# Performance work log

Measured on AMD Instinct MI355X. Metric: run time of the kernel, lower is better.

The kernel has to match this reference:

```python
import jax, jax.numpy as jnp
import numpy as np

NEG = -1e30  # log-space 'zero'


def _lse3(a, b, c):
    # numerically stable logsumexp of three [B,L] arrays, NEG acts as -inf
    m = jnp.maximum(jnp.maximum(a, b), c)
    valid = m > NEG / 2
    m_safe = jnp.where(valid, m, 0.0)
    s = jnp.exp(a - m_safe) + jnp.exp(b - m_safe) + jnp.exp(c - m_safe)
    # add 1 where invalid so log() stays finite (result is masked anyway)
    return jnp.where(valid, m_safe + jnp.log(s + (~valid)), NEG)


def _lse2(a, b):
    m = jnp.maximum(a, b)
    valid = m > NEG / 2
    m_safe = jnp.where(valid, m, 0.0)
    s = jnp.exp(a - m_safe) + jnp.exp(b - m_safe)
    return jnp.where(valid, m_safe + jnp.log(s + (~valid)), NEG)


def ctc_loss(log_probs, targets, input_lengths, target_lengths):
    # log_probs: [T,B,C] already log-softmaxed; blank=0; reduction='mean'; zero_infinity
    T, B, C = log_probs.shape
    S = targets.shape[0] // B  # equal target lengths -> reshape concatenated targets
    tgt = targets.reshape(B, S)
    L = 2 * S + 1
    # extended label sequence: blank, l1, blank, l2, ..., blank
    ext = jnp.zeros((B, L), dtype=tgt.dtype).at[:, 1::2].set(tgt)
    # emissions gathered at extended labels: [T,B,L]
    emit = log_probs[:, jnp.arange(B)[:, None], ext]

    # skip transition (l-2 -> l) allowed iff ext[l] != blank and ext[l] != ext[l-2]
    skip_ok = jnp.concatenate(
        [jnp.zeros((B, 2), bool), (ext[:, 2:] != 0) & (ext[:, 2:] != ext[:, :-2])],
        axis=1,
    )

    def shift(a, n):
        return jnp.pad(a, ((0, 0), (n, 0)), constant_values=NEG)[:, :L]

    alpha0 = (
        jnp.full((B, L), NEG, log_probs.dtype)
        .at[:, 0].set(emit[0, :, 0])
        .at[:, 1].set(emit[0, :, 1])
    )

    def step(alpha, xs):
        t, emit_t = xs
        a1 = shift(alpha, 1)
        a2 = jnp.where(skip_ok, shift(alpha, 2), NEG)
        new = _lse3(alpha, a1, a2) + emit_t
        # freeze alpha once past each sample's input length
        new = jnp.where((t < input_lengths)[:, None], new, alpha)
        return new, None

    alpha, _ = jax.lax.scan(step, alpha0, (jnp.arange(1, T), emit[1:]))

    b_idx = jnp.arange(B)
    hi = 2 * target_lengths  # last blank position
    ll = _lse2(alpha[b_idx, hi], alpha[b_idx, hi - 1])
    loss = jnp.where(ll > NEG / 2, -ll, 0.0)  # zero_infinity=True
    return jnp.mean(loss / target_lengths.astype(log_probs.dtype))


def setup_inputs() -> dict:
    key = jax.random.key(0)
    k1, k2 = jax.random.split(key)
    T, B, C, S = 1024, 128, 256, 64
    logits = jax.random.normal(k1, (T, B, C), jnp.float32)
    log_probs = jax.nn.log_softmax(logits, axis=-1)
    targets = jax.random.randint(k2, (B * S,), 1, C)  # blank=0 excluded
    input_lengths = jnp.full((B,), T, jnp.int32)
    target_lengths = jnp.full((B,), S, jnp.int32)
    return {
        "log_probs": log_probs,
        "targets": targets,
        "input_lengths": input_lengths,
        "target_lengths": target_lengths,
    }


def reference(log_probs, targets, input_lengths, target_lengths):
    return ctc_loss(log_probs, targets, input_lengths, target_lengths)
```

## Files before the change

kernel.cpp:

```cpp
#include <hip/hip_runtime.h>


#define NEGV (-1e30f)
#define NEGH (-5e29f)

constexpr int T_  = 1024;
constexpr int C_  = 256;
constexpr int CH  = 64;
constexpr int NCH = T_ / CH;

__device__ __forceinline__ float lse2f(float x, float y) {
    float m = fmaxf(x, y);
    float s = __expf(x - m) + __expf(y - m);
    float r = m + __logf(s);
    return (m > NEGH) ? r : NEGV;
}

__device__ __forceinline__ float fshr1(float x) {
    int i = __float_as_int(x);
    int p = __builtin_amdgcn_update_dpp(0, i, 0x138, 0xf, 0xf, false);
    return __int_as_float(p);
}

template <int CTRL>
__device__ __forceinline__ int dpp_imaxstep(int x) {
    int r = __builtin_amdgcn_update_dpp(x, x, CTRL, 0xf, 0xf, false);
    return max(x, r);
}

#define PDECL(S) float S##g0,S##g1,S##g2,S##g3,S##g4,S##g5,S##g6,S##g7, \
                       S##l0,S##l1,S##l2,S##l3,S##l4,S##l5,S##l6,S##l7
#define PLOAD1(S,J,TB) { int t_ = (TB) + J; t_ = t_ > 1023 ? 1023 : t_;      \
    const float* rp_ = rowb + (size_t)t_ * BC;                               \
    S##g##J = rp_[my_tgt]; S##l##J = rp_[0]; }
#define PLOAD(S,TB) PLOAD1(S,0,TB) PLOAD1(S,1,TB) PLOAD1(S,2,TB)             \
                    PLOAD1(S,3,TB) PLOAD1(S,4,TB) PLOAD1(S,5,TB)             \
                    PLOAD1(S,6,TB) PLOAD1(S,7,TB)
#define PSTORE1(S,J,RB,BUFP) BUFP[((RB) + J) * 64 + lane] =                  \
    make_float2(__expf(S##g##J), __expf(S##l##J));
#define PSTORE(S,RB,BUFP) PSTORE1(S,0,RB,BUFP) PSTORE1(S,1,RB,BUFP)          \
                          PSTORE1(S,2,RB,BUFP) PSTORE1(S,3,RB,BUFP)          \
                          PSTORE1(S,4,RB,BUFP) PSTORE1(S,5,RB,BUFP)          \
                          PSTORE1(S,6,RB,BUFP) PSTORE1(S,7,RB,BUFP)
#define LOADCHUNK(T0) PLOAD(A,(T0)) PLOAD(Bx,(T0)+8)                         \
                      PLOAD(Cx,(T0)+16) PLOAD(Dx,(T0)+24)
#define STORECHUNK(RB,BUFP) PSTORE(A,(RB),BUFP) PSTORE(Bx,(RB)+8,BUFP)       \
                            PSTORE(Cx,(RB)+16,BUFP) PSTORE(Dx,(RB)+24,BUFP)

__global__ __launch_bounds__(192) void ctc_alpha_kernel(
    const float* __restrict__ lp,
    const int* __restrict__ targets,
    const int* __restrict__ in_len,
    const int* __restrict__ tgt_len,
    float* __restrict__ partial,
    int B, int S)
{
    __shared__ float2 stage[2][CH * 64];
    __shared__ float sh[132];

    const int b    = blockIdx.x;
    const int tid  = threadIdx.x;
    const int wave = tid >> 6;
    const int lane = tid & 63;
    const int BC   = B * C_;
    const float* rowb = lp + (size_t)b * C_;

    int my_tgt = (lane < S) ? targets[b * S + lane] : 0;
    int prev_tgt = __shfl_up(my_tgt, 1);
    const bool skip = (lane > 0) && (my_tgt != prev_tgt) && (my_tgt != 0);
    const float skipf = skip ? 1.f : 0.f;
    const int ilen = in_len[b];

    float pa = 0.f, pb = 0.f, pc = 0.f;
    int es = 0;

    PDECL(A); PDECL(Bx); PDECL(Cx); PDECL(Dx);
    const int r0 = (wave - 1) * 32;

    if (wave >= 1) {
        LOADCHUNK(1 + r0);
        { float2* bp = &stage[0][0]; STORECHUNK(r0, bp); }
        LOADCHUNK(1 + CH + r0);
    } else if (lane == 0) {
        pa = __expf(rowb[0]);
        pb = __expf(rowb[my_tgt]);
    }
    __syncthreads();

#define STEP(cur) {                                                          \
        float eml = (cur).x;                                                 \
        float ebl = (cur).y;                                                 \
        float pprev = fshr1(pb);                                \
        float t0s = pa + pb;                               \
        float nb = fmaf(skipf, pprev, t0s) * eml;            \
        float na = (pa + pprev) * ebl;                       \
        float nc = (pc + pb) * ebl;                          \
        pa = na; pb = nb; pc = nc; }

#define RESCALE() {                                                          \
        int h = __float_as_int(fmaxf(fmaxf(pa, pb), pc));                    \
        h = dpp_imaxstep<0x111>(h);                         \
        h = dpp_imaxstep<0x112>(h);                         \
        h = dpp_imaxstep<0x114>(h);                         \
        h = dpp_imaxstep<0x118>(h);                         \
        h = dpp_imaxstep<0x142>(h);                         \
        h = dpp_imaxstep<0x143>(h);                         \
        int hm = __builtin_amdgcn_readlane(h, 63);                           \
        int e = ((hm >> 23) & 0xff) - 127;                                   \
        pa = ldexpf(pa, -e); pb = ldexpf(pb, -e); pc = ldexpf(pc, -e);       \
        es += e; }

    for (int kc = 0; kc < NCH; ++kc) {
        if (wave >= 1) {
            if (kc + 1 < NCH) {
                float2* bp = &stage[(kc + 1) & 1][0];
                STORECHUNK(r0, bp);
            }
            if (kc + 2 < NCH) {
                LOADCHUNK(1 + (kc + 2) * CH + r0);
            }
        } else {
            const int t0 = 1 + kc * CH;
            const float2* sb = &stage[kc & 1][lane];
            if (t0 + CH <= ilen) {
                float2 f0 = sb[0 * 64];
                float2 f1 = sb[1 * 64];
                float2 f2 = sb[2 * 64];
                float2 f3 = sb[3 * 64];
#pragma unroll
                for (int r = 0; r < CH; ++r) {
                    float2 cur = f0;
                    f0 = f1; f1 = f2; f2 = f3;
                    if (r + 4 < CH) f3 = sb[(r + 4) * 64];
                    STEP(cur);
                    if ((r & 7) == 7) RESCALE();
                }
            } else if (t0 < ilen) {
                float2 f0 = sb[0 * 64];
                float2 f1 = sb[1 * 64];
                float2 f2 = sb[2 * 64];
                float2 f3 = sb[3 * 64];
#pragma unroll
                for (int r = 0; r < CH; ++r) {
                    float2 cur = f0;
                    f0 = f1; f1 = f2; f2 = f3;
                    if (r + 4 < CH) f3 = sb[(r + 4) * 64];
                    if (t0 + r < ilen) {
                        STEP(cur);
                        if ((r & 7) == 7) RESCALE();
                    }
                }
            }
        }
        __syncthreads();
    }

    if (wave == 0) {
        const double lses = (double)es * 0.6931471805599453;
        auto logp = [&](float p) -> float {
            if (p == 0.f) return NEGV;
            float q = p * 33554432.0f;
            if (q == 0.f) return NEGV;
            int h = __float_as_int(q);
            int E = ((h >> 23) & 0xff) - 127 - 25;
            float m = __int_as_float((h & 0x807fffff) | (127 << 23));
            return (float)(__logf(m) + ((double)E * 0.6931471805599453 + lses));
        };
        sh[2 * lane]     = logp(pa);
        sh[2 * lane + 1] = logp(pb);
        if (lane == 63) sh[128] = logp(pc);
    }
    __syncthreads();
    if (tid == 0) {
        int tl = tgt_len[b];
        int hi2 = 2 * tl;
        float ll = lse2f(sh[hi2], sh[hi2 - 1]);
        float loss = (ll > NEGH) ? -ll : 0.f;
        partial[b] = loss / (float)tl;
    }
}

__global__ __launch_bounds__(128) void ctc_reduce_kernel(
    const float* __restrict__ partial, float* __restrict__ out, int B)
{
    float v = 0.f;
    for (int j = threadIdx.x; j < B; j += 128) v += partial[j];
#pragma unroll
    for (int off = 32; off > 0; off >>= 1)
        v += __shfl_down(v, off);
    __shared__ float ws[2];
    if ((threadIdx.x & 63) == 0) ws[threadIdx.x >> 6] = v;
    __syncthreads();
    if (threadIdx.x == 0) out[0] = (ws[0] + ws[1]) / (float)B;
}

extern "C" void kernel_launch(void* const* d_in, const int* in_sizes, int n_in,
                              void* d_out, int out_size, void* d_ws, size_t ws_size,
                              hipStream_t stream)
{
    const float* lp      = (const float*)d_in[0];
    const int*   targets = (const int*)d_in[1];
    const int*   il      = (const int*)d_in[2];
    const int*   tl      = (const int*)d_in[3];
    const int B = in_sizes[2];
    const int S = in_sizes[1] / B;

    float* partial = (float*)d_ws;

    ctc_alpha_kernel<<<B, 192, 0, stream>>>(lp, targets, il, tl, partial, B, S);
    ctc_reduce_kernel<<<1, 128, 0, stream>>>(partial, (float*)d_out, B);
}
```

Baseline: 195.1 us.

## Use per-lane scale exponents instead of wave-wide max rescaling

Replaces the wave-wide max reduction (six DPP max steps plus readlane) in the periodic rescale with a per-lane exponent normalization. Each lane keeps its own scale exponent. Every step it shifts the neighbour's exponent with DPP and adjusts the incoming neighbour value via ldexp by the exponent difference, and it adopts the neighbour's exponent when its own state is zero. This takes the cross-lane reduction off the rescale path but adds a DPP, a compare and an ldexp to every recurrence step, and the final log conversion still uses the now per-lane es.

```diff
diff --git a/kernel.cpp b/kernel.cpp
--- a/kernel.cpp
+++ b/kernel.cpp
@@ -14,18 +14,6 @@
     float s = __expf(x - m) + __expf(y - m);
     float r = m + __logf(s);
     return (m > NEGH) ? r : NEGV;
-}
-
-__device__ __forceinline__ float fshr1(float x) {
-    int i = __float_as_int(x);
-    int p = __builtin_amdgcn_update_dpp(0, i, 0x138, 0xf, 0xf, false);
-    return __int_as_float(p);
-}
-
-template <int CTRL>
-__device__ __forceinline__ int dpp_imaxstep(int x) {
-    int r = __builtin_amdgcn_update_dpp(x, x, CTRL, 0xf, 0xf, false);
-    return max(x, r);
 }
 
 #define PDECL(S) float S##g0,S##g1,S##g2,S##g3,S##g4,S##g5,S##g6,S##g7, \
@@ -90,25 +78,25 @@
 #define STEP(cur) {                                                          \
         float eml = (cur).x;                                                 \
         float ebl = (cur).y;                                                 \
-        float pprev = fshr1(pb);                                \
-        float t0s = pa + pb;                               \
+        int praw = __builtin_amdgcn_update_dpp(0, __float_as_int(pb),        \
+                                               0x138, 0xf, 0xf, false);      \
+        int esp  = __builtin_amdgcn_update_dpp(0, es,                        \
+                                               0x138, 0xf, 0xf, false);      \
+        bool dead = (fmaxf(fmaxf(pa, pb), pc) == 0.f);                       \
+        es = dead ? esp : es;          \
+        int des = min(esp - es, 64);                                         \
+        float pprev = ldexpf(__int_as_float(praw), des);        \
+        float t0s = pa + pb;                                                 \
         float nb = fmaf(skipf, pprev, t0s) * eml;            \
         float na = (pa + pprev) * ebl;                       \
         float nc = (pc + pb) * ebl;                          \
         pa = na; pb = nb; pc = nc; }
 
 #define RESCALE() {                                                          \
-        int h = __float_as_int(fmaxf(fmaxf(pa, pb), pc));                    \
-        h = dpp_imaxstep<0x111>(h);                         \
-        h = dpp_imaxstep<0x112>(h);                         \
-        h = dpp_imaxstep<0x114>(h);                         \
-        h = dpp_imaxstep<0x118>(h);                         \
-        h = dpp_imaxstep<0x142>(h);                         \
-        h = dpp_imaxstep<0x143>(h);                         \
-        int hm = __builtin_amdgcn_readlane(h, 63);                           \
-        int e = ((hm >> 23) & 0xff) - 127;                                   \
-        pa = ldexpf(pa, -e); pb = ldexpf(pb, -e); pc = ldexpf(pc, -e);       \
-        es += e; }
+        int hb = __float_as_int(fmaxf(fmaxf(pa, pb), pc));                   \
+        int sh_ = hb ? (159 - (hb >> 23)) : 0;                   \
+        pa = ldexpf(pa, sh_); pb = ldexpf(pb, sh_); pc = ldexpf(pc, sh_);    \
+        es -= sh_; }
 
     for (int kc = 0; kc < NCH; ++kc) {
         if (wave >= 1) {
```

Result: no change. 197.5 us (+1.2%).
